# Performance work log

Measured on AMD Instinct MI355X. Metric: run time of the kernel, lower is better.

Reference implementation:

```python
import jax, jax.numpy as jnp
import numpy as np

# Synthetic NEAT-style layered DAG (matches init_kwargs)
N_IN = 512      # input nodes
L = 5           # computed layers (last = outputs)
M = 2048        # nodes per computed layer
FAN = 32        # incoming edges per computed node
B = 1024        # batch size
N = N_IN + L * M        # total nodes
E = M * FAN             # edges per layer (grouped by destination layer)


def setup_inputs() -> dict:
    rng = np.random.default_rng(0)
    src = np.zeros((L, E), np.int32)
    dst = np.zeros((L, E), np.int32)
    for l in range(L):
        prefix = N_IN + l * M  # edges may come from any earlier node (DAG w/ skips)
        src[l] = rng.integers(0, prefix, size=E)
        dst[l] = np.repeat(np.arange(M, dtype=np.int32), FAN)
    key = jax.random.key(0)
    k1, k2, k3 = jax.random.split(key, 3)
    x = jax.random.normal(k1, (B, N_IN), jnp.float32)
    weights = jax.random.normal(k2, (L, E), jnp.float32) * 0.1
    biases = jax.random.normal(k3, (L, M), jnp.float32) * 0.01
    return {
        "x": x,
        "weights": weights,
        "biases": biases,
        "src_idx": jnp.asarray(src),
        "dst_idx": jnp.asarray(dst),
    }


def reference(x, weights, biases, src_idx, dst_idx):
    b = x.shape[0]
    # values[:, node] as in the torch module; inputs copied in first
    vals = jnp.zeros((b, N), x.dtype).at[:, :N_IN].set(x)
    for l in range(L):  # topological layers (fixed, small count)
        # gather source activations for this layer's edges and weight them
        contrib = vals[:, src_idx[l]] * weights[l]                    # [B, E]
        # scatter-add into destination nodes of this layer
        layer = jnp.zeros((b, M), x.dtype).at[:, dst_idx[l]].add(contrib)
        layer = jax.nn.relu(layer + biases[l])
        vals = vals.at[:, N_IN + l * M : N_IN + (l + 1) * M].set(layer)
    # output nodes = last computed layer
    return vals[:, N_IN + (L - 1) * M :]
```

## Files before the change

kernel.cpp:

```cpp
#include <hip/hip_runtime.h>

#define N_IN    512
#define NLAYERS 5
#define M_NODES 2048
#define FAN     32
#define B_BATCH 1024
#define E_EDGES (M_NODES * FAN)
#define N_TOTAL (N_IN + NLAYERS * M_NODES)

#define CB      4
#define NBLK    (B_BATCH / CB)
#define GROUPS  (M_NODES / 64)
#define ECH     (FAN / 4)
#define LDS_BYTES (N_TOTAL * 8)

typedef unsigned short u16;
typedef unsigned int   u32;

__device__ __forceinline__ u16 f2bf(float f) {
    u32 b = __float_as_uint(f);
    return (u16)((b + 0x7FFFu + ((b >> 16) & 1u)) >> 16);
}

__global__ __launch_bounds__(1024) void pack_edges(
    const float* __restrict__ w,
    const int* __restrict__ src,
    u32* __restrict__ pck) {
    const int d = blockIdx.x * 1024 + threadIdx.x;
    if (d >= NLAYERS * E_EDGES) return;
    const int l    = d >> 16;
    const int r    = d & 65535;
    const int g    = r >> 11;
    const int ec   = (r & 2047) >> 8;
    const int lane = (r & 255) >> 2;
    const int c    = r & 3;
    const int j = g * 64 + lane;
    const int k = ec * 4 + c;
    const size_t e = (size_t)l * E_EDGES + j * FAN + k;
    pck[d] = ((u32)f2bf(w[e]) << 16) | (u32)(u16)src[e];
}

__global__ __launch_bounds__(1024) void net_kernel(
    const float* __restrict__ x,
    const u32* __restrict__ pck,
    const float* __restrict__ bias,
    float* __restrict__ out) {
    extern __shared__ u32 vals[];
    uint2* vals2 = reinterpret_cast<uint2*>(vals);

    const int t   = threadIdx.x;
    const int blk = blockIdx.x;
    const int lane6 = t & 63;

    if (t < N_IN) {
        const float v0 = x[(size_t)(4 * blk + 0) * N_IN + t];
        const float v1 = x[(size_t)(4 * blk + 1) * N_IN + t];
        const float v2 = x[(size_t)(4 * blk + 2) * N_IN + t];
        const float v3 = x[(size_t)(4 * blk + 3) * N_IN + t];
        vals2[t] = make_uint2((u32)f2bf(v0) | ((u32)f2bf(v1) << 16),
                              (u32)f2bf(v2) | ((u32)f2bf(v3) << 16));
    }

    for (int l = 0; l < NLAYERS; ++l) {
        __syncthreads();
        const int base = N_IN + l * M_NODES;
#pragma unroll
        for (int r = 0; r < 2; ++r) {
            const int j = r * 1024 + t;
            const int g = j >> 6;
            const uint4* ep = reinterpret_cast<const uint4*>(pck) +
                              ((size_t)((l * GROUPS + g) * ECH) * 64 + lane6);
            const float bj = bias[l * M_NODES + j];
            float a0 = bj, a1 = bj, a2 = bj, a3 = bj;
#pragma unroll
            for (int ec = 0; ec < ECH; ++ec) {
                const uint4 wd = ep[(size_t)ec * 64];
                const u32 words[4] = {wd.x, wd.y, wd.z, wd.w};
#pragma unroll
                for (int c = 0; c < 4; ++c) {
                    const u32 word = words[c];
                    const u32 s    = word & 0xFFFFu;
                    const float wv = __uint_as_float(word & 0xFFFF0000u);
                    const uint2 v  = vals2[s];
                    a0 = fmaf(wv, __uint_as_float(v.x << 16),          a0);
                    a1 = fmaf(wv, __uint_as_float(v.x & 0xFFFF0000u), a1);
                    a2 = fmaf(wv, __uint_as_float(v.y << 16),          a2);
                    a3 = fmaf(wv, __uint_as_float(v.y & 0xFFFF0000u), a3);
                }
            }
            a0 = fmaxf(a0, 0.f);
            a1 = fmaxf(a1, 0.f);
            a2 = fmaxf(a2, 0.f);
            a3 = fmaxf(a3, 0.f);
            if (l < NLAYERS - 1) {
                vals2[base + j] =
                    make_uint2((u32)f2bf(a0) | ((u32)f2bf(a1) << 16),
                               (u32)f2bf(a2) | ((u32)f2bf(a3) << 16));
            } else {
                out[(size_t)(4 * blk + 0) * M_NODES + j] = a0;
                out[(size_t)(4 * blk + 1) * M_NODES + j] = a1;
                out[(size_t)(4 * blk + 2) * M_NODES + j] = a2;
                out[(size_t)(4 * blk + 3) * M_NODES + j] = a3;
            }
        }
    }
}

extern "C" void kernel_launch(void* const* d_in, const int* in_sizes, int n_in,
                              void* d_out, int out_size, void* d_ws, size_t ws_size,
                              hipStream_t stream) {
    const float* x       = (const float*)d_in[0];
    const float* weights = (const float*)d_in[1];
    const float* biases  = (const float*)d_in[2];
    const int*   src_idx = (const int*)d_in[3];
    float* out = (float*)d_out;
    u32*   pck = (u32*)d_ws;

    pack_edges<<<(NLAYERS * E_EDGES + 1023) / 1024, 1024, 0, stream>>>(
        weights, src_idx, pck);

    static bool attr_done = [] {
        hipFuncSetAttribute(reinterpret_cast<const void*>(net_kernel),
                            hipFuncAttributeMaxDynamicSharedMemorySize,
                            LDS_BYTES);
        return true;
    }();
    (void)attr_done;
    hipFuncSetAttribute(reinterpret_cast<const void*>(net_kernel),
                        hipFuncAttributeMaxDynamicSharedMemorySize, LDS_BYTES);
    net_kernel<<<NBLK, 1024, LDS_BYTES, stream>>>(x, pck, biases, out);
}
```

Before: 90.52 us.

## Halve batch rows per block to shrink LDS and pack edges as pairs

Each block now processes 2 batch rows instead of 4, storing two bf16 activations per node in a 32-bit word. This halves the LDS footprint to about 42KB of static shared memory, so two blocks can share a CU instead of one. The edge packing changes to uint2 pairs to match. The trade-off is twice as many blocks, each re-reading the full packed edge stream, so global/L2 traffic for weights and indices doubles and gather work per edge is amortized over fewer rows.

```diff
diff --git a/kernel.cpp b/kernel.cpp
--- a/kernel.cpp
+++ b/kernel.cpp
@@ -8,11 +8,10 @@
 #define E_EDGES (M_NODES * FAN)
 #define N_TOTAL (N_IN + NLAYERS * M_NODES)
 
-#define CB      4
+#define CB      2
 #define NBLK    (B_BATCH / CB)
 #define GROUPS  (M_NODES / 64)
-#define ECH     (FAN / 4)
-#define LDS_BYTES (N_TOTAL * 8)
+#define ECH     (FAN / 2)
 
 typedef unsigned short u16;
 typedef unsigned int   u32;
@@ -31,34 +30,32 @@
     const int l    = d >> 16;
     const int r    = d & 65535;
     const int g    = r >> 11;
-    const int ec   = (r & 2047) >> 8;
-    const int lane = (r & 255) >> 2;
-    const int c    = r & 3;
+    const int rem  = r & 2047;
+    const int ec   = rem >> 7;
+    const int lane = (rem >> 1) & 63;
+    const int c    = rem & 1;
     const int j = g * 64 + lane;
-    const int k = ec * 4 + c;
+    const int k = ec * 2 + c;
     const size_t e = (size_t)l * E_EDGES + j * FAN + k;
     pck[d] = ((u32)f2bf(w[e]) << 16) | (u32)(u16)src[e];
 }
 
-__global__ __launch_bounds__(1024) void net_kernel(
+__global__ __launch_bounds__(1024, 8) void net_kernel(
     const float* __restrict__ x,
     const u32* __restrict__ pck,
     const float* __restrict__ bias,
     float* __restrict__ out) {
-    extern __shared__ u32 vals[];
-    uint2* vals2 = reinterpret_cast<uint2*>(vals);
+    __shared__ u32 vals[N_TOTAL];
 
     const int t   = threadIdx.x;
     const int blk = blockIdx.x;
-    const int lane6 = t & 63;
+    const int b0  = 2 * blk;
+    const int b1  = 2 * blk + 1;
 
     if (t < N_IN) {
-        const float v0 = x[(size_t)(4 * blk + 0) * N_IN + t];
-        const float v1 = x[(size_t)(4 * blk + 1) * N_IN + t];
-        const float v2 = x[(size_t)(4 * blk + 2) * N_IN + t];
-        const float v3 = x[(size_t)(4 * blk + 3) * N_IN + t];
-        vals2[t] = make_uint2((u32)f2bf(v0) | ((u32)f2bf(v1) << 16),
-                              (u32)f2bf(v2) | ((u32)f2bf(v3) << 16));
+        const float v0 = x[(size_t)b0 * N_IN + t];
+        const float v1 = x[(size_t)b1 * N_IN + t];
+        vals[t] = (u32)f2bf(v0) | ((u32)f2bf(v1) << 16);
     }
 
     for (int l = 0; l < NLAYERS; ++l) {
@@ -66,41 +63,33 @@
         const int base = N_IN + l * M_NODES;
 #pragma unroll
         for (int r = 0; r < 2; ++r) {
-            const int j = r * 1024 + t;
-            const int g = j >> 6;
-            const uint4* ep = reinterpret_cast<const uint4*>(pck) +
-                              ((size_t)((l * GROUPS + g) * ECH) * 64 + lane6);
+            const int j     = r * 1024 + t;
+            const int g     = j >> 6;
+            const int lane6 = j & 63;
+            const uint2* ep = reinterpret_cast<const uint2*>(pck) +
+                              ((size_t)(l * GROUPS + g) * ECH) * 64 + lane6;
             const float bj = bias[l * M_NODES + j];
-            float a0 = bj, a1 = bj, a2 = bj, a3 = bj;
+            float a0 = bj, a1 = bj;
 #pragma unroll
             for (int ec = 0; ec < ECH; ++ec) {
-                const uint4 wd = ep[(size_t)ec * 64];
-                const u32 words[4] = {wd.x, wd.y, wd.z, wd.w};
+                const uint2 wd = ep[(size_t)ec * 64];
 #pragma unroll
-                for (int c = 0; c < 4; ++c) {
-                    const u32 word = words[c];
+                for (int c = 0; c < 2; ++c) {
+                    const u32 word = (c == 0) ? wd.x : wd.y;
                     const u32 s    = word & 0xFFFFu;
                     const float wv = __uint_as_float(word & 0xFFFF0000u);
-                    const uint2 v  = vals2[s];
-                    a0 = fmaf(wv, __uint_as_float(v.x << 16),          a0);
-                    a1 = fmaf(wv, __uint_as_float(v.x & 0xFFFF0000u), a1);
-                    a2 = fmaf(wv, __uint_as_float(v.y << 16),          a2);
-                    a3 = fmaf(wv, __uint_as_float(v.y & 0xFFFF0000u), a3);
+                    const u32 v    = vals[s];
+                    a0 = fmaf(wv, __uint_as_float(v << 16),          a0);
+                    a1 = fmaf(wv, __uint_as_float(v & 0xFFFF0000u),  a1);
                 }
             }
             a0 = fmaxf(a0, 0.f);
             a1 = fmaxf(a1, 0.f);
-            a2 = fmaxf(a2, 0.f);
-            a3 = fmaxf(a3, 0.f);
             if (l < NLAYERS - 1) {
-                vals2[base + j] =
-                    make_uint2((u32)f2bf(a0) | ((u32)f2bf(a1) << 16),
-                               (u32)f2bf(a2) | ((u32)f2bf(a3) << 16));
+                vals[base + j] = (u32)f2bf(a0) | ((u32)f2bf(a1) << 16);
             } else {
-                out[(size_t)(4 * blk + 0) * M_NODES + j] = a0;
-                out[(size_t)(4 * blk + 1) * M_NODES + j] = a1;
-                out[(size_t)(4 * blk + 2) * M_NODES + j] = a2;
-                out[(size_t)(4 * blk + 3) * M_NODES + j] = a3;
+                out[(size_t)b0 * M_NODES + j] = a0;
+                out[(size_t)b1 * M_NODES + j] = a1;
             }
         }
     }
@@ -119,14 +108,5 @@
     pack_edges<<<(NLAYERS * E_EDGES + 1023) / 1024, 1024, 0, stream>>>(
         weights, src_idx, pck);
 
-    static bool attr_done = [] {
-        hipFuncSetAttribute(reinterpret_cast<const void*>(net_kernel),
-                            hipFuncAttributeMaxDynamicSharedMemorySize,
-                            LDS_BYTES);
-        return true;
-    }();
-    (void)attr_done;
-    hipFuncSetAttribute(reinterpret_cast<const void*>(net_kernel),
-                        hipFuncAttributeMaxDynamicSharedMemorySize, LDS_BYTES);
-    net_kernel<<<NBLK, 1024, LDS_BYTES, stream>>>(x, pck, biases, out);
+    net_kernel<<<NBLK, 1024, 0, stream>>>(x, pck, biases, out);
 }
```

After: 128.7 us. 42.2% more time.

## Reorder per-node edges to spread LDS banks, shrink LDS, prefetch edge words

Applied to the files above, without the earlier changes.

The pack kernel now handles one node per thread. It groups each node's 32 edges by the low 4 bits of the source index and rotates the slots by node id, so lanes reading LDS at the same step hit different banks. LDS is cut to the prefix actually read (the last layer is never stored), which could let more blocks fit per CU. The main loop also software-prefetches the next uint4 of edge words. The reordered pack kernel does scattered writes and serial per-thread loops, which adds preprocessing cost.

```diff
diff --git a/kernel.cpp b/kernel.cpp
--- a/kernel.cpp
+++ b/kernel.cpp
@@ -7,12 +7,13 @@
 #define B_BATCH 1024
 #define E_EDGES (M_NODES * FAN)
 #define N_TOTAL (N_IN + NLAYERS * M_NODES)
+#define PREFIX4 (N_IN + 4 * M_NODES)
 
 #define CB      4
 #define NBLK    (B_BATCH / CB)
 #define GROUPS  (M_NODES / 64)
 #define ECH     (FAN / 4)
-#define LDS_BYTES (N_TOTAL * 8)
+#define NODES_ALL (NLAYERS * M_NODES)
 
 typedef unsigned short u16;
 typedef unsigned int   u32;
@@ -22,22 +23,44 @@
     return (u16)((b + 0x7FFFu + ((b >> 16) & 1u)) >> 16);
 }
 
-__global__ __launch_bounds__(1024) void pack_edges(
+__global__ __launch_bounds__(256) void pack_edges(
     const float* __restrict__ w,
     const int* __restrict__ src,
     u32* __restrict__ pck) {
-    const int d = blockIdx.x * 1024 + threadIdx.x;
-    if (d >= NLAYERS * E_EDGES) return;
-    const int l    = d >> 16;
-    const int r    = d & 65535;
-    const int g    = r >> 11;
-    const int ec   = (r & 2047) >> 8;
-    const int lane = (r & 255) >> 2;
-    const int c    = r & 3;
-    const int j = g * 64 + lane;
-    const int k = ec * 4 + c;
-    const size_t e = (size_t)l * E_EDGES + j * FAN + k;
-    pck[d] = ((u32)f2bf(w[e]) << 16) | (u32)(u16)src[e];
+    const int n = blockIdx.x * 256 + threadIdx.x;
+    if (n >= NODES_ALL) return;
+    const int l = n >> 11;
+    const int j = n & (M_NODES - 1);
+
+    u32 words[FAN];
+    int cnt[16];
+#pragma unroll
+    for (int i = 0; i < 16; ++i) cnt[i] = 0;
+
+    const size_t eb = (size_t)l * E_EDGES + (size_t)j * FAN;
+#pragma unroll 1
+    for (int k = 0; k < FAN; ++k) {
+        const int s = src[eb + k];
+        words[k] = ((u32)f2bf(w[eb + k]) << 16) | (u32)(s & 0xFFFF);
+        cnt[s & 15]++;
+    }
+    int startp[16];
+    int acc = 0;
+#pragma unroll
+    for (int i = 0; i < 16; ++i) { startp[i] = acc; acc += cnt[i]; }
+
+    const int g    = j >> 6;
+    const int lane = j & 63;
+    const int rot  = j & 31;
+    const size_t nb = (size_t)(l * GROUPS + g) * ECH;
+#pragma unroll 1
+    for (int k = 0; k < FAN; ++k) {
+        const u32 wd  = words[k];
+        const int key = wd & 15;
+        const int r   = startp[key]++;
+        const int kp  = (r + rot) & 31;
+        pck[((nb + (kp >> 2)) * 64 + lane) * 4 + (kp & 3)] = wd;
+    }
 }
 
 __global__ __launch_bounds__(1024) void net_kernel(
@@ -45,18 +68,16 @@
     const u32* __restrict__ pck,
     const float* __restrict__ bias,
     float* __restrict__ out) {
-    extern __shared__ u32 vals[];
-    uint2* vals2 = reinterpret_cast<uint2*>(vals);
+    __shared__ uint2 vals2[PREFIX4];
 
     const int t   = threadIdx.x;
     const int blk = blockIdx.x;
-    const int lane6 = t & 63;
 
     if (t < N_IN) {
-        const float v0 = x[(size_t)(4 * blk + 0) * N_IN + t];
-        const float v1 = x[(size_t)(4 * blk + 1) * N_IN + t];
-        const float v2 = x[(size_t)(4 * blk + 2) * N_IN + t];
-        const float v3 = x[(size_t)(4 * blk + 3) * N_IN + t];
+        const float v0 = x[(size_t)(CB * blk + 0) * N_IN + t];
+        const float v1 = x[(size_t)(CB * blk + 1) * N_IN + t];
+        const float v2 = x[(size_t)(CB * blk + 2) * N_IN + t];
+        const float v3 = x[(size_t)(CB * blk + 3) * N_IN + t];
         vals2[t] = make_uint2((u32)f2bf(v0) | ((u32)f2bf(v1) << 16),
                               (u32)f2bf(v2) | ((u32)f2bf(v3) << 16));
     }
@@ -66,19 +87,22 @@
         const int base = N_IN + l * M_NODES;
 #pragma unroll
         for (int r = 0; r < 2; ++r) {
-            const int j = r * 1024 + t;
-            const int g = j >> 6;
+            const int j     = r * 1024 + t;
+            const int g     = j >> 6;
+            const int lane6 = j & 63;
             const uint4* ep = reinterpret_cast<const uint4*>(pck) +
-                              ((size_t)((l * GROUPS + g) * ECH) * 64 + lane6);
+                              (size_t)(l * GROUPS + g) * ECH * 64 + lane6;
             const float bj = bias[l * M_NODES + j];
             float a0 = bj, a1 = bj, a2 = bj, a3 = bj;
+
+            uint4 wd = ep[0];
 #pragma unroll
             for (int ec = 0; ec < ECH; ++ec) {
-                const uint4 wd = ep[(size_t)ec * 64];
-                const u32 words[4] = {wd.x, wd.y, wd.z, wd.w};
+                const uint4 nxt = (ec < ECH - 1) ? ep[(ec + 1) * 64] : wd;
 #pragma unroll
                 for (int c = 0; c < 4; ++c) {
-                    const u32 word = words[c];
+                    const u32 word = (c == 0) ? wd.x : (c == 1) ? wd.y
+                                    : (c == 2) ? wd.z : wd.w;
                     const u32 s    = word & 0xFFFFu;
                     const float wv = __uint_as_float(word & 0xFFFF0000u);
                     const uint2 v  = vals2[s];
@@ -87,6 +111,7 @@
                     a2 = fmaf(wv, __uint_as_float(v.y << 16),          a2);
                     a3 = fmaf(wv, __uint_as_float(v.y & 0xFFFF0000u), a3);
                 }
+                wd = nxt;
             }
             a0 = fmaxf(a0, 0.f);
             a1 = fmaxf(a1, 0.f);
@@ -97,10 +122,10 @@
                     make_uint2((u32)f2bf(a0) | ((u32)f2bf(a1) << 16),
                                (u32)f2bf(a2) | ((u32)f2bf(a3) << 16));
             } else {
-                out[(size_t)(4 * blk + 0) * M_NODES + j] = a0;
-                out[(size_t)(4 * blk + 1) * M_NODES + j] = a1;
-                out[(size_t)(4 * blk + 2) * M_NODES + j] = a2;
-                out[(size_t)(4 * blk + 3) * M_NODES + j] = a3;
+                out[(size_t)(CB * blk + 0) * M_NODES + j] = a0;
+                out[(size_t)(CB * blk + 1) * M_NODES + j] = a1;
+                out[(size_t)(CB * blk + 2) * M_NODES + j] = a2;
+                out[(size_t)(CB * blk + 3) * M_NODES + j] = a3;
             }
         }
     }
@@ -116,17 +141,8 @@
     float* out = (float*)d_out;
     u32*   pck = (u32*)d_ws;
 
-    pack_edges<<<(NLAYERS * E_EDGES + 1023) / 1024, 1024, 0, stream>>>(
+    pack_edges<<<(NODES_ALL + 255) / 256, 256, 0, stream>>>(
         weights, src_idx, pck);
 
-    static bool attr_done = [] {
-        hipFuncSetAttribute(reinterpret_cast<const void*>(net_kernel),
-                            hipFuncAttributeMaxDynamicSharedMemorySize,
-                            LDS_BYTES);
-        return true;
-    }();
-    (void)attr_done;
-    hipFuncSetAttribute(reinterpret_cast<const void*>(net_kernel),
-                        hipFuncAttributeMaxDynamicSharedMemorySize, LDS_BYTES);
-    net_kernel<<<NBLK, 1024, LDS_BYTES, stream>>>(x, pck, biases, out);
+    net_kernel<<<NBLK, 1024, 0, stream>>>(x, pck, biases, out);
 }
```

New measurement: 107.0 us. 18.2% more time.
